# Optimization experiments

Measured on AMD Instinct MI355X. Metric: run time of the kernel, lower is better.

## Reference

```python
import jax, jax.numpy as jnp
import numpy as np

B, T, C = 4, 2048, 1024
H, D = 16, 64


def setup_inputs() -> dict:
    key = jax.random.key(0)
    ks = jax.random.split(key, 5)
    x = jax.random.normal(ks[0], (B, T, C), dtype=jnp.float32)
    Wq = jax.random.normal(ks[1], (H, C, D), dtype=jnp.float32) * (C ** -0.5)
    Wk = jax.random.normal(ks[2], (H, C, D), dtype=jnp.float32) * (C ** -0.5)
    Wv = jax.random.normal(ks[3], (H, C, D), dtype=jnp.float32) * (C ** -0.5)
    Wp = jax.random.normal(ks[4], (H * D, C), dtype=jnp.float32) * ((H * D) ** -0.5)
    bp = jnp.zeros((C,), dtype=jnp.float32)
    return {"x": x, "Wq": Wq, "Wk": Wk, "Wv": Wv, "Wp": Wp, "bp": bp}


def reference(x, Wq, Wk, Wv, Wp, bp):
    # per-head projections (bias-free): [B,H,T,D]
    q = jnp.einsum('btc,hcd->bhtd', x, Wq)
    k = jnp.einsum('btc,hcd->bhtd', x, Wk)
    v = jnp.einsum('btc,hcd->bhtd', x, Wv)
    # NOTE: source multiplies by sqrt(head_size) (faithful to original code)
    scale = jnp.asarray(D ** 0.5, x.dtype)
    att = jnp.einsum('bhtd,bhsd->bhts', q, k) * scale  # [B,H,T,T]
    causal = jnp.tril(jnp.ones((T, T), dtype=bool))
    att = jnp.where(causal, att, jnp.asarray(-jnp.inf, att.dtype))
    att = jax.nn.softmax(att, axis=-1)
    out = jnp.einsum('bhts,bhsd->bhtd', att, v)  # [B,H,T,D]
    out = out.transpose(0, 2, 1, 3).reshape(B, T, H * D)  # head concat
    return out @ Wp + bp
```

## Files before the change

kernel.cpp:

```cpp
#include <hip/hip_runtime.h>

#define B_ 4
#define T_ 2048
#define C_ 1024
#define H_ 16
#define D_ 64

typedef _Float16 f16x8 __attribute__((ext_vector_type(8)));
typedef __fp16 fp16x2 __attribute__((ext_vector_type(2)));
typedef float f32x4 __attribute__((ext_vector_type(4)));
typedef unsigned short u16x8 __attribute__((ext_vector_type(8)));

#define MFMA16 __builtin_amdgcn_mfma_f32_16x16x32_f16
#define SCALE2 11.541560327111707f

__device__ __forceinline__ unsigned pk2(float a, float b) {
    fp16x2 p = __builtin_amdgcn_cvt_pkrtz(a, b);
    return __builtin_bit_cast(unsigned, p);
}

__device__ __forceinline__ void gl_lds16(const _Float16* g, unsigned short* lds) {
    __builtin_amdgcn_global_load_lds(
        (const __attribute__((address_space(1))) unsigned int*)g,
        (__attribute__((address_space(3))) unsigned int*)lds, 16, 0, 0);
}

__global__ __launch_bounds__(256) void convx_kernel(const float* __restrict__ x,
                                                    _Float16* __restrict__ Xf) {
    size_t i = ((size_t)blockIdx.x * 256 + threadIdx.x) * 8;
    f32x4 a = *reinterpret_cast<const f32x4*>(x + i);
    f32x4 b = *reinterpret_cast<const f32x4*>(x + i + 4);
    f16x8 o;
    o[0] = (_Float16)a[0]; o[1] = (_Float16)a[1]; o[2] = (_Float16)a[2]; o[3] = (_Float16)a[3];
    o[4] = (_Float16)b[0]; o[5] = (_Float16)b[1]; o[6] = (_Float16)b[2]; o[7] = (_Float16)b[3];
    *reinterpret_cast<f16x8*>(Xf + i) = o;
}

__global__ __launch_bounds__(256) void convw_qkv_kernel(
    const float* __restrict__ Wq, const float* __restrict__ Wk, const float* __restrict__ Wv,
    _Float16* __restrict__ Wqt, _Float16* __restrict__ Wkt, _Float16* __restrict__ Wvt)
{
    __shared__ unsigned short Wl[128][72];
    const int ct = blockIdx.x, h = blockIdx.y, m = blockIdx.z;
    const float* src = (m == 0 ? Wq : (m == 1 ? Wk : Wv)) + ((size_t)h * C_ + ct * 128) * D_;
    _Float16* dst = (m == 0 ? Wqt : (m == 1 ? Wkt : Wvt));
    const int tid = threadIdx.x;
    {
        int r = tid >> 1, half = tid & 1;
        #pragma unroll
        for (int i = 0; i < 8; i++) {
            f32x4 v = *reinterpret_cast<const f32x4*>(src + (size_t)r * D_ + half * 32 + i * 4);
            #pragma unroll
            for (int j = 0; j < 4; j++)
                Wl[r][half * 32 + i * 4 + j] = __builtin_bit_cast(unsigned short, (_Float16)v[j]);
        }
    }
    __syncthreads();
    {
        int d = tid >> 2, seg = tid & 3;
        #pragma unroll
        for (int i = 0; i < 4; i++) {
            u16x8 o;
            #pragma unroll
            for (int j = 0; j < 8; j++) o[j] = Wl[seg * 32 + i * 8 + j][d];
            *reinterpret_cast<u16x8*>((unsigned short*)dst + ((size_t)h * D_ + d) * C_ + ct * 128 + seg * 32 + i * 8) = o;
        }
    }
}

__global__ __launch_bounds__(256) void convw_p_kernel(const float* __restrict__ Wp,
                                                      _Float16* __restrict__ Wpt)
{
    __shared__ unsigned short Pl[64][72];
    const int jt = blockIdx.x, kt = blockIdx.y;
    const int tid = threadIdx.x;
    {
        int r = tid >> 2, seg = tid & 3;
        #pragma unroll
        for (int i = 0; i < 4; i++) {
            f32x4 v = *reinterpret_cast<const f32x4*>(Wp + (size_t)(kt * 64 + r) * C_ + jt * 64 + seg * 16 + i * 4);
            #pragma unroll
            for (int j = 0; j < 4; j++)
                Pl[r][seg * 16 + i * 4 + j] = __builtin_bit_cast(unsigned short, (_Float16)v[j]);
        }
    }
    __syncthreads();
    {
        int jj = tid >> 2, kseg = tid & 3;
        #pragma unroll
        for (int i = 0; i < 2; i++) {
            u16x8 o;
            #pragma unroll
            for (int j = 0; j < 8; j++) o[j] = Pl[kseg * 16 + i * 8 + j][jj];
            *reinterpret_cast<u16x8*>((unsigned short*)Wpt + (size_t)(jt * 64 + jj) * C_ + kt * 64 + kseg * 16 + i * 8) = o;
        }
    }
}

__global__ __launch_bounds__(256) void qkv4_kernel(
    const _Float16* __restrict__ Xf, const _Float16* __restrict__ Wcat,
    _Float16* __restrict__ Qf, _Float16* __restrict__ Kf, _Float16* __restrict__ Vt)
{
    __shared__ unsigned short As[128 * 64];
    __shared__ unsigned short Bs[192 * 64];
    const int rt = blockIdx.x, ct = blockIdx.y;
    const int row0 = rt * 128, n0 = ct * 192;
    const int tid = threadIdx.x, wid = tid >> 6, lane = tid & 63;
    const int l15 = lane & 15, g = lane >> 4;
    const int wr = wid >> 1, wc = wid & 1;
    const int lrow = lane >> 3, lcol = (lane & 7) * 8;

    f32x4 acc[4][6];
    #pragma unroll
    for (int mi = 0; mi < 4; mi++)
        #pragma unroll
        for (int ni = 0; ni < 6; ni++) { f32x4 z = {0.f,0.f,0.f,0.f}; acc[mi][ni] = z; }

    for (int k0 = 0; k0 < C_; k0 += 64) {
        __syncthreads();
        #pragma unroll
        for (int i = 0; i < 4; i++) {
            int c = wid * 4 + i;
            gl_lds16(Xf + (size_t)(row0 + c * 8 + lrow) * C_ + k0 + lcol, &As[c * 512]);
        }
        #pragma unroll
        for (int i = 0; i < 6; i++) {
            int c = wid * 6 + i;
            gl_lds16(Wcat + (size_t)(n0 + c * 8 + lrow) * C_ + k0 + lcol, &Bs[c * 512]);
        }
        __syncthreads();
        #pragma unroll
        for (int kk = 0; kk < 2; kk++) {
            f16x8 af[4];
            #pragma unroll
            for (int mi = 0; mi < 4; mi++)
                af[mi] = *reinterpret_cast<const f16x8*>(&As[(wr * 64 + mi * 16 + l15) * 64 + kk * 32 + g * 8]);
            #pragma unroll
            for (int ni = 0; ni < 6; ni++) {
                f16x8 bf = *reinterpret_cast<const f16x8*>(&Bs[(wc * 96 + ni * 16 + l15) * 64 + kk * 32 + g * 8]);
                #pragma unroll
                for (int mi = 0; mi < 4; mi++)
                    acc[mi][ni] = MFMA16(af[mi], bf, acc[mi][ni], 0, 0, 0);
            }
        }
    }

    const int b = row0 >> 11;
    const int t0b = (row0 & (T_ - 1)) + wr * 64;
    #pragma unroll
    for (int ni = 0; ni < 6; ni++) {
        const int n = n0 + wc * 96 + ni * 16;
        const int region = n >> 10;
        const int h = (n >> 6) & 15;
        const int d0 = n & 63;
        if (region < 2) {
            _Float16* dst = region ? Kf : Qf;
            const float osc = region ? 1.0f : SCALE2;
            const size_t hb = ((size_t)(b * H_ + h)) * T_ * D_;
            #pragma unroll
            for (int mi = 0; mi < 4; mi++)
                #pragma unroll
                for (int r = 0; r < 4; r++) {
                    int t = t0b + mi * 16 + g * 4 + r;
                    dst[hb + (size_t)t * D_ + d0 + l15] = (_Float16)(acc[mi][ni][r] * osc);
                }
        } else {
            const size_t vbase = ((size_t)(b * H_ + h)) * D_ * T_;
            const int d = d0 + l15;
            #pragma unroll
            for (int mi = 0; mi < 4; mi++) {
                int t = t0b + mi * 16 + g * 4;
                uint2 w;
                w.x = pk2(acc[mi][ni][0], acc[mi][ni][1]);
                w.y = pk2(acc[mi][ni][2], acc[mi][ni][3]);
                *reinterpret_cast<uint2*>((unsigned short*)Vt + vbase + (size_t)d * T_ + t) = w;
            }
        }
    }
}

__global__ __launch_bounds__(256) void flash_kernel(
    const _Float16* __restrict__ Qf, const _Float16* __restrict__ Kf,
    const _Float16* __restrict__ Vt, _Float16* __restrict__ att)
{
    __shared__ __align__(16) unsigned short Ks[2][64 * 64];
    __shared__ __align__(16) unsigned short Vs[2][64 * 64];
    __shared__ __align__(16) unsigned short Ps[4][32 * 32];
    const int bh = blockIdx.x;
    const int p = (int)blockIdx.y;
    const int bb = bh >> 4, h = bh & 15;
    const int tid = threadIdx.x, wid = tid >> 6, lane = tid & 63;
    const int l15 = lane & 15, g = lane >> 4;

    const _Float16* Qb = Qf + (size_t)bh * T_ * D_;
    const _Float16* Kb = Kf + (size_t)bh * T_ * D_;
    const _Float16* Vb = Vt + (size_t)bh * D_ * T_;

    const int srow = lane >> 3;
    const int sunit = (lane & 7) ^ srow;
    const int r0s = wid * 16;

    char* const pbase = (char*)&Ps[wid][0];

    for (int pass = 0; pass < 2; pass++) {
        const int qt = pass ? p : (15 - p);
        const int q0 = qt * 128;
        const int qw = q0 + wid * 32;

        f16x8 qf[2][2];
        #pragma unroll
        for (int mt = 0; mt < 2; mt++)
            #pragma unroll
            for (int kk = 0; kk < 2; kk++)
                qf[mt][kk] = *reinterpret_cast<const f16x8*>(Qb + (size_t)(qw + mt * 16 + l15) * D_ + kk * 32 + g * 8);

        f32x4 accO[4][2];
        #pragma unroll
        for (int nt = 0; nt < 4; nt++)
            #pragma unroll
            for (int mt = 0; mt < 2; mt++) { f32x4 z = {0.f,0.f,0.f,0.f}; accO[nt][mt] = z; }
        float m[2] = { -1e30f, -1e30f };
        float l[2] = { 0.f, 0.f };

        const int myNt = (qw + 95) >> 6;
        const int ntB  = (q0 + 191) >> 6;

        #pragma unroll
        for (int i = 0; i < 2; i++) {
            int row = r0s + i * 8 + srow;
            gl_lds16(Kb + (size_t)row * D_ + sunit * 8, &Ks[0][(r0s + i * 8) * 64]);
            gl_lds16(Vb + (size_t)row * T_ + sunit * 8, &Vs[0][(r0s + i * 8) * 64]);
        }
        __syncthreads();

#define TILE_BODY(TI, BUF)                                                          \
    {                                                                               \
        const int kv0 = (TI) * 64;                                                  \
        if ((TI) + 1 < ntB) {                                                       \
            const int kvn = kv0 + 64;                                               \
            _Pragma("unroll")                                                       \
            for (int i = 0; i < 2; i++) {                                           \
                int row = r0s + i * 8 + srow;                                       \
                gl_lds16(Kb + (size_t)(kvn + row) * D_ + sunit * 8,                 \
                         &Ks[(BUF) ^ 1][(r0s + i * 8) * 64]);                       \
                gl_lds16(Vb + (size_t)row * T_ + kvn + sunit * 8,                   \
                         &Vs[(BUF) ^ 1][(r0s + i * 8) * 64]);                       \
            }                                                                       \
        }                                                                           \
        if ((TI) < myNt) {                                                          \
            const bool maskt = ((TI) == myNt - 1);                                  \
            const char* kbase = (const char*)&Ks[BUF][0];                           \
            const char* vbase = (const char*)&Vs[BUF][0];                           \
            f32x4 s[4][2];                                                          \
            _Pragma("unroll")                                                       \
            for (int st = 0; st < 4; st++)                                          \
                _Pragma("unroll")                                                   \
                for (int mt = 0; mt < 2; mt++) { f32x4 z = {0.f,0.f,0.f,0.f}; s[st][mt] = z; } \
            _Pragma("unroll")                                                       \
            for (int kk = 0; kk < 2; kk++) {                                        \
                f16x8 kfr[4];                                                       \
                _Pragma("unroll")                                                   \
                for (int st = 0; st < 4; st++) {                                    \
                    int row = st * 16 + l15;                                        \
                    kfr[st] = *reinterpret_cast<const f16x8*>(                      \
                        kbase + row * 128 + (((kk * 4 + g) ^ (row & 7)) * 16));     \
                }                                                                   \
                _Pragma("unroll")                                                   \
                for (int st = 0; st < 4; st++)                                      \
                    _Pragma("unroll")                                               \
                    for (int mt = 0; mt < 2; mt++)                                  \
                        s[st][mt] = MFMA16(kfr[st], qf[mt][kk], s[st][mt], 0, 0, 0);\
            }                                                                       \
            unsigned pw[2][4][2];                                                   \
            _Pragma("unroll")                                                       \
            for (int mt = 0; mt < 2; mt++) {                                        \
                const int r = mt * 16 + l15;                                        \
                const int qrow = qw + r;                                            \
                float lv[4][4];                                                     \
                float vmax = -1e30f;                                                \
                _Pragma("unroll")                                                   \
                for (int st = 0; st < 4; st++)                                      \
                    _Pragma("unroll")                                               \
                    for (int rr = 0; rr < 4; rr++) {                                \
                        float v = s[st][mt][rr];                                    \
                        if (maskt) {                                                \
                            int kv = kv0 + st * 16 + g * 4 + rr;                    \
                            v = (kv <= qrow) ? v : -1e30f;                          \
                        }                                                           \
                        lv[st][rr] = v;                                             \
                        vmax = fmaxf(vmax, v);                                      \
                    }                                                               \
                vmax = fmaxf(vmax, __shfl_xor(vmax, 16, 64));                       \
                vmax = fmaxf(vmax, __shfl_xor(vmax, 32, 64));                       \
                float mnew = fmaxf(m[mt], vmax);                                    \
                float alpha = __builtin_amdgcn_exp2f(m[mt] - mnew);                 \
                m[mt] = mnew;                                                       \
                float rs = 0.f;                                                     \
                _Pragma("unroll")                                                   \
                for (int st = 0; st < 4; st++) {                                    \
                    float p0 = __builtin_amdgcn_exp2f(lv[st][0] - mnew);            \
                    float p1 = __builtin_amdgcn_exp2f(lv[st][1] - mnew);            \
                    float p2 = __builtin_amdgcn_exp2f(lv[st][2] - mnew);            \
                    float p3 = __builtin_amdgcn_exp2f(lv[st][3] - mnew);            \
                    rs += (p0 + p1) + (p2 + p3);                                    \
                    pw[mt][st][0] = pk2(p0, p1);                                    \
                    pw[mt][st][1] = pk2(p2, p3);                                    \
                }                                                                   \
                rs += __shfl_xor(rs, 16, 64);                                       \
                rs += __shfl_xor(rs, 32, 64);                                       \
                l[mt] = l[mt] * alpha + rs;                                         \
                _Pragma("unroll")                                                   \
                for (int nt = 0; nt < 4; nt++) accO[nt][mt] *= alpha;               \
            }                                                                       \
            _Pragma("unroll")                                                       \
            for (int half = 0; half < 2; half++) {                                  \
                _Pragma("unroll")                                                   \
                for (int mt = 0; mt < 2; mt++) {                                    \
                    const int r = mt * 16 + l15;                                    \
                    const int swz = ((r >> 1) & 3) << 4;                            \
                    char* prow = pbase + r * 64;                                    \
                    _Pragma("unroll")                                               \
                    for (int stl = 0; stl < 2; stl++) {                             \
                        uint2 w;                                                    \
                        w.x = pw[mt][half * 2 + stl][0];                            \
                        w.y = pw[mt][half * 2 + stl][1];                            \
                        *reinterpret_cast<uint2*>(prow + ((stl * 32 + g * 8) ^ swz)) = w; \
                    }                                                               \
                }                                                                   \
                f16x8 pb[2];                                                        \
                _Pragma("unroll")                                                   \
                for (int mt = 0; mt < 2; mt++) {                                    \
                    const int r = mt * 16 + l15;                                    \
                    const int swz = ((r >> 1) & 3) << 4;                            \
                    pb[mt] = *reinterpret_cast<const f16x8*>(pbase + r * 64 + ((g * 16) ^ swz)); \
                }                                                                   \
                _Pragma("unroll")                                                   \
                for (int nt = 0; nt < 4; nt++) {                                    \
                    int row = nt * 16 + l15;                                        \
                    f16x8 vf = *reinterpret_cast<const f16x8*>(                     \
                        vbase + row * 128 + (((half * 4 + g) ^ (row & 7)) * 16));   \
                    _Pragma("unroll")                                               \
                    for (int mt = 0; mt < 2; mt++)                                  \
                        accO[nt][mt] = MFMA16(vf, pb[mt], accO[nt][mt], 0, 0, 0);   \
                }                                                                   \
            }                                                                       \
        }                                                                           \
        __syncthreads();                                                            \
    }

        for (int tI = 0; tI < ntB; tI += 2) {
            TILE_BODY(tI, 0)
            if (tI + 1 < ntB) {
                TILE_BODY(tI + 1, 1)
            }
        }
#undef TILE_BODY

        #pragma unroll
        for (int mt = 0; mt < 2; mt++) {
            float inv = 1.0f / l[mt];
            int t = qw + mt * 16 + l15;
            #pragma unroll
            for (int nt = 0; nt < 4; nt++) {
                f32x4 o = accO[nt][mt] * inv;
                uint2 w;
                w.x = pk2(o[0], o[1]);
                w.y = pk2(o[2], o[3]);
                size_t off = ((size_t)(bb * T_ + t)) * (H_ * D_) + h * D_ + nt * 16 + g * 4;
                *reinterpret_cast<uint2*>((unsigned short*)att + off) = w;
            }
        }
    }
}

__global__ __launch_bounds__(256) void proj2_kernel(
    const _Float16* __restrict__ att, const _Float16* __restrict__ Wpt,
    const float* __restrict__ bp, float* __restrict__ out)
{
    __shared__ unsigned short As[128 * 64];
    __shared__ unsigned short Bs[128 * 64];
    const int rt = blockIdx.x, ct = blockIdx.y;
    const int row0 = rt * 128, n0 = ct * 128;
    const int tid = threadIdx.x, wid = tid >> 6, lane = tid & 63;
    const int l15 = lane & 15, g = lane >> 4;
    const int wr = wid >> 1, wc = wid & 1;
    const int lrow = lane >> 3, lcol = (lane & 7) * 8;

    f32x4 acc[4][4];
    #pragma unroll
    for (int mi = 0; mi < 4; mi++)
        #pragma unroll
        for (int ni = 0; ni < 4; ni++) { f32x4 z = {0.f,0.f,0.f,0.f}; acc[mi][ni] = z; }

    for (int k0 = 0; k0 < C_; k0 += 64) {
        __syncthreads();
        #pragma unroll
        for (int i = 0; i < 4; i++) {
            int c = wid * 4 + i;
            gl_lds16(att + (size_t)(row0 + c * 8 + lrow) * C_ + k0 + lcol, &As[c * 512]);
            gl_lds16(Wpt + (size_t)(n0   + c * 8 + lrow) * C_ + k0 + lcol, &Bs[c * 512]);
        }
        __syncthreads();
        #pragma unroll
        for (int kk = 0; kk < 2; kk++) {
            f16x8 af[4], bf[4];
            #pragma unroll
            for (int mi = 0; mi < 4; mi++)
                af[mi] = *reinterpret_cast<const f16x8*>(&As[(wr * 64 + mi * 16 + l15) * 64 + kk * 32 + g * 8]);
            #pragma unroll
            for (int ni = 0; ni < 4; ni++)
                bf[ni] = *reinterpret_cast<const f16x8*>(&Bs[(wc * 64 + ni * 16 + l15) * 64 + kk * 32 + g * 8]);
            #pragma unroll
            for (int mi = 0; mi < 4; mi++)
                #pragma unroll
                for (int ni = 0; ni < 4; ni++)
                    acc[mi][ni] = MFMA16(af[mi], bf[ni], acc[mi][ni], 0, 0, 0);
        }
    }

    #pragma unroll
    for (int mi = 0; mi < 4; mi++)
        #pragma unroll
        for (int ni = 0; ni < 4; ni++) {
            int col = n0 + wc * 64 + ni * 16 + l15;
            float bias = bp[col];
            #pragma unroll
            for (int r = 0; r < 4; r++) {
                int row = row0 + wr * 64 + mi * 16 + g * 4 + r;
                out[(size_t)row * C_ + col] = acc[mi][ni][r] + bias;
            }
        }
}

extern "C" void kernel_launch(void* const* d_in, const int* in_sizes, int n_in,
                              void* d_out, int out_size, void* d_ws, size_t ws_size,
                              hipStream_t stream) {
    const float* x  = (const float*)d_in[0];
    const float* Wq = (const float*)d_in[1];
    const float* Wk = (const float*)d_in[2];
    const float* Wv = (const float*)d_in[3];
    const float* Wp = (const float*)d_in[4];
    const float* bp = (const float*)d_in[5];
    float* out = (float*)d_out;

    _Float16* Xf  = (_Float16*)d_ws;
    _Float16* Wqt = Xf  + (size_t)8388608;
    _Float16* Wkt = Wqt + (size_t)1048576;
    _Float16* Wvt = Wkt + (size_t)1048576;
    _Float16* Wpt = Wvt + (size_t)1048576;
    _Float16* Qf  = Wpt + (size_t)1048576;
    _Float16* Kf  = Qf  + (size_t)8388608;
    _Float16* Vt  = Kf  + (size_t)8388608;
    _Float16* att = Vt  + (size_t)8388608;

    convx_kernel<<<4096, 256, 0, stream>>>(x, Xf);
    convw_qkv_kernel<<<dim3(8, 16, 3), 256, 0, stream>>>(Wq, Wk, Wv, Wqt, Wkt, Wvt);
    convw_p_kernel<<<dim3(16, 16), 256, 0, stream>>>(Wp, Wpt);
    qkv4_kernel<<<dim3(64, 16), 256, 0, stream>>>(Xf, Wqt, Qf, Kf, Vt);
    flash_kernel<<<dim3(64, 8), 256, 0, stream>>>(Qf, Kf, Vt, att);
    proj2_kernel<<<dim3(64, 8), 256, 0, stream>>>(att, Wpt, bp, out);
}
```

Measured before the change: 195.5 us.

## Shrink flash query tile to 64 rows, doubling grid for more parallelism

The flash attention block now covers 64 query rows, one 16-row MFMA tile per wave, instead of 128 rows with two tiles per wave. The grid doubles to 64x16 with paired causal tiles (31-j and j), which raises block count and lowers register use per wave to improve occupancy and load balance. In exchange, each K/V tile loaded into LDS is reused by half as many query rows, so K/V traffic per unit of work doubles. The per-wave skip of fully masked KV tiles is removed because all waves now share the same tile count.

```diff
diff --git a/kernel.cpp b/kernel.cpp
--- a/kernel.cpp
+++ b/kernel.cpp
@@ -185,9 +185,9 @@
 {
     __shared__ __align__(16) unsigned short Ks[2][64 * 64];
     __shared__ __align__(16) unsigned short Vs[2][64 * 64];
-    __shared__ __align__(16) unsigned short Ps[4][32 * 32];
+    __shared__ __align__(16) unsigned short Ps[4][16 * 32];
     const int bh = blockIdx.x;
-    const int p = (int)blockIdx.y;
+    const int j = (int)blockIdx.y;
     const int bb = bh >> 4, h = bh & 15;
     const int tid = threadIdx.x, wid = tid >> 6, lane = tid & 63;
     const int l15 = lane & 15, g = lane >> 4;
@@ -201,29 +201,27 @@
     const int r0s = wid * 16;
 
     char* const pbase = (char*)&Ps[wid][0];
+    const int r = l15;
+    const int swz = ((r >> 1) & 3) << 4;
 
     for (int pass = 0; pass < 2; pass++) {
-        const int qt = pass ? p : (15 - p);
-        const int q0 = qt * 128;
-        const int qw = q0 + wid * 32;
-
-        f16x8 qf[2][2];
-        #pragma unroll
-        for (int mt = 0; mt < 2; mt++)
-            #pragma unroll
-            for (int kk = 0; kk < 2; kk++)
-                qf[mt][kk] = *reinterpret_cast<const f16x8*>(Qb + (size_t)(qw + mt * 16 + l15) * D_ + kk * 32 + g * 8);
-
-        f32x4 accO[4][2];
-        #pragma unroll
-        for (int nt = 0; nt < 4; nt++)
-            #pragma unroll
-            for (int mt = 0; mt < 2; mt++) { f32x4 z = {0.f,0.f,0.f,0.f}; accO[nt][mt] = z; }
-        float m[2] = { -1e30f, -1e30f };
-        float l[2] = { 0.f, 0.f };
-
-        const int myNt = (qw + 95) >> 6;
-        const int ntB  = (q0 + 191) >> 6;
+        const int s = pass ? j : (31 - j);
+        const int q0 = s * 64;
+        const int qw = q0 + wid * 16;
+        const int qrow = qw + r;
+
+        f16x8 qf[2];
+        #pragma unroll
+        for (int kk = 0; kk < 2; kk++)
+            qf[kk] = *reinterpret_cast<const f16x8*>(Qb + (size_t)(qw + l15) * D_ + kk * 32 + g * 8);
+
+        f32x4 accO[4];
+        #pragma unroll
+        for (int nt = 0; nt < 4; nt++) { f32x4 z = {0.f,0.f,0.f,0.f}; accO[nt] = z; }
+        float m = -1e30f;
+        float l = 0.f;
+
+        const int ntB = s + 1;
 
         #pragma unroll
         for (int i = 0; i < 2; i++) {
@@ -247,15 +245,13 @@
                          &Vs[(BUF) ^ 1][(r0s + i * 8) * 64]);                       \
             }                                                                       \
         }                                                                           \
-        if ((TI) < myNt) {                                                          \
-            const bool maskt = ((TI) == myNt - 1);                                  \
+        {                                                                           \
+            const bool maskt = ((TI) == ntB - 1);                                   \
             const char* kbase = (const char*)&Ks[BUF][0];                           \
             const char* vbase = (const char*)&Vs[BUF][0];                           \
-            f32x4 s[4][2];                                                          \
-            _Pragma("unroll")                                                       \
-            for (int st = 0; st < 4; st++)                                          \
-                _Pragma("unroll")                                                   \
-                for (int mt = 0; mt < 2; mt++) { f32x4 z = {0.f,0.f,0.f,0.f}; s[st][mt] = z; } \
+            f32x4 s4[4];                                                            \
+            _Pragma("unroll")                                                       \
+            for (int st = 0; st < 4; st++) { f32x4 z = {0.f,0.f,0.f,0.f}; s4[st] = z; } \
             _Pragma("unroll")                                                       \
             for (int kk = 0; kk < 2; kk++) {                                        \
                 f16x8 kfr[4];                                                       \
@@ -267,81 +263,61 @@
                 }                                                                   \
                 _Pragma("unroll")                                                   \
                 for (int st = 0; st < 4; st++)                                      \
-                    _Pragma("unroll")                                               \
-                    for (int mt = 0; mt < 2; mt++)                                  \
-                        s[st][mt] = MFMA16(kfr[st], qf[mt][kk], s[st][mt], 0, 0, 0);\
+                    s4[st] = MFMA16(kfr[st], qf[kk], s4[st], 0, 0, 0);              \
             }                                                                       \
-            unsigned pw[2][4][2];                                                   \
-            _Pragma("unroll")                                                       \
-            for (int mt = 0; mt < 2; mt++) {                                        \
-                const int r = mt * 16 + l15;                                        \
-                const int qrow = qw + r;                                            \
-                float lv[4][4];                                                     \
-                float vmax = -1e30f;                                                \
+            float lv[4][4];                                                         \
+            float vmax = -1e30f;                                                    \
+            _Pragma("unroll")                                                       \
+            for (int st = 0; st < 4; st++)                                          \
                 _Pragma("unroll")                                                   \
-                for (int st = 0; st < 4; st++)                                      \
-                    _Pragma("unroll")                                               \
-                    for (int rr = 0; rr < 4; rr++) {                                \
-                        float v = s[st][mt][rr];                                    \
-                        if (maskt) {                                                \
-                            int kv = kv0 + st * 16 + g * 4 + rr;                    \
-                            v = (kv <= qrow) ? v : -1e30f;                          \
-                        }                                                           \
-                        lv[st][rr] = v;                                             \
-                        vmax = fmaxf(vmax, v);                                      \
+                for (int rr = 0; rr < 4; rr++) {                                    \
+                    float v = s4[st][rr];                                           \
+                    if (maskt) {                                                    \
+                        int kv = kv0 + st * 16 + g * 4 + rr;                        \
+                        v = (kv <= qrow) ? v : -1e30f;                              \
                     }                                                               \
-                vmax = fmaxf(vmax, __shfl_xor(vmax, 16, 64));                       \
-                vmax = fmaxf(vmax, __shfl_xor(vmax, 32, 64));                       \
-                float mnew = fmaxf(m[mt], vmax);                                    \
-                float alpha = __builtin_amdgcn_exp2f(m[mt] - mnew);                 \
-                m[mt] = mnew;                                                       \
-                float rs = 0.f;                                                     \
-                _Pragma("unroll")                                                   \
-                for (int st = 0; st < 4; st++) {                                    \
-                    float p0 = __builtin_amdgcn_exp2f(lv[st][0] - mnew);            \
-                    float p1 = __builtin_amdgcn_exp2f(lv[st][1] - mnew);            \
-                    float p2 = __builtin_amdgcn_exp2f(lv[st][2] - mnew);            \
-                    float p3 = __builtin_amdgcn_exp2f(lv[st][3] - mnew);            \
-                    rs += (p0 + p1) + (p2 + p3);                                    \
-                    pw[mt][st][0] = pk2(p0, p1);                                    \
-                    pw[mt][st][1] = pk2(p2, p3);                                    \
+                    lv[st][rr] = v;                                                 \
+                    vmax = fmaxf(vmax, v);                                          \
                 }                                                                   \
-                rs += __shfl_xor(rs, 16, 64);                                       \
-                rs += __shfl_xor(rs, 32, 64);                                       \
-                l[mt] = l[mt] * alpha + rs;                                         \
-                _Pragma("unroll")                                                   \
-                for (int nt = 0; nt < 4; nt++) accO[nt][mt] *= alpha;               \
+            vmax = fmaxf(vmax, __shfl_xor(vmax, 16, 64));                           \
+            vmax = fmaxf(vmax, __shfl_xor(vmax, 32, 64));                           \
+            float mnew = fmaxf(m, vmax);                                            \
+            float alpha = __builtin_amdgcn_exp2f(m - mnew);                         \
+            m = mnew;                                                               \
+            float rs = 0.f;                                                         \
+            unsigned pw[4][2];                                                      \
+            _Pragma("unroll")                                                       \
+            for (int st = 0; st < 4; st++) {                                        \
+                float p0 = __builtin_amdgcn_exp2f(lv[st][0] - mnew);                \
+                float p1 = __builtin_amdgcn_exp2f(lv[st][1] - mnew);                \
+                float p2 = __builtin_amdgcn_exp2f(lv[st][2] - mnew);                \
+                float p3 = __builtin_amdgcn_exp2f(lv[st][3] - mnew);                \
+                rs += (p0 + p1) + (p2 + p3);                                        \
+                pw[st][0] = pk2(p0, p1);                                            \
+                pw[st][1] = pk2(p2, p3);                                            \
             }                                                                       \
+            rs += __shfl_xor(rs, 16, 64);                                           \
+            rs += __shfl_xor(rs, 32, 64);                                           \
+            l = l * alpha + rs;                                                     \
+            _Pragma("unroll")                                                       \
+            for (int nt = 0; nt < 4; nt++) accO[nt] *= alpha;                       \
+            char* prow = pbase + r * 64;                                            \
             _Pragma("unroll")                                                       \
             for (int half = 0; half < 2; half++) {                                  \
                 _Pragma("unroll")                                                   \
-                for (int mt = 0; mt < 2; mt++) {                                    \
-                    const int r = mt * 16 + l15;                                    \
-                    const int swz = ((r >> 1) & 3) << 4;                            \
-                    char* prow = pbase + r * 64;                                    \
-                    _Pragma("unroll")                                               \
-                    for (int stl = 0; stl < 2; stl++) {                             \
-                        uint2 w;                                                    \
-                        w.x = pw[mt][half * 2 + stl][0];                            \
-                        w.y = pw[mt][half * 2 + stl][1];                            \
-                        *reinterpret_cast<uint2*>(prow + ((stl * 32 + g * 8) ^ swz)) = w; \
-                    }                                                               \
+                for (int stl = 0; stl < 2; stl++) {                                 \
+                    uint2 w;                                                        \
+                    w.x = pw[half * 2 + stl][0];                                    \
+                    w.y = pw[half * 2 + stl][1];                                    \
+                    *reinterpret_cast<uint2*>(prow + ((stl * 32 + g * 8) ^ swz)) = w; \
                 }                                                                   \
-                f16x8 pb[2];                                                        \
-                _Pragma("unroll")                                                   \
-                for (int mt = 0; mt < 2; mt++) {                                    \
-                    const int r = mt * 16 + l15;                                    \
-                    const int swz = ((r >> 1) & 3) << 4;                            \
-                    pb[mt] = *reinterpret_cast<const f16x8*>(pbase + r * 64 + ((g * 16) ^ swz)); \
-                }                                                                   \
+                f16x8 pb = *reinterpret_cast<const f16x8*>(prow + ((g * 16) ^ swz)); \
                 _Pragma("unroll")                                                   \
                 for (int nt = 0; nt < 4; nt++) {                                    \
                     int row = nt * 16 + l15;                                        \
                     f16x8 vf = *reinterpret_cast<const f16x8*>(                     \
                         vbase + row * 128 + (((half * 4 + g) ^ (row & 7)) * 16));   \
-                    _Pragma("unroll")                                               \
-                    for (int mt = 0; mt < 2; mt++)                                  \
-                        accO[nt][mt] = MFMA16(vf, pb[mt], accO[nt][mt], 0, 0, 0);   \
+                    accO[nt] = MFMA16(vf, pb, accO[nt], 0, 0, 0);                   \
                 }                                                                   \
             }                                                                       \
         }                                                                           \
@@ -356,13 +332,12 @@
         }
 #undef TILE_BODY
 
-        #pragma unroll
-        for (int mt = 0; mt < 2; mt++) {
-            float inv = 1.0f / l[mt];
-            int t = qw + mt * 16 + l15;
+        {
+            float inv = 1.0f / l;
+            int t = qw + l15;
             #pragma unroll
             for (int nt = 0; nt < 4; nt++) {
-                f32x4 o = accO[nt][mt] * inv;
+                f32x4 o = accO[nt] * inv;
                 uint2 w;
                 w.x = pk2(o[0], o[1]);
                 w.y = pk2(o[2], o[3]);
@@ -457,6 +432,6 @@
     convw_qkv_kernel<<<dim3(8, 16, 3), 256, 0, stream>>>(Wq, Wk, Wv, Wqt, Wkt, Wvt);
     convw_p_kernel<<<dim3(16, 16), 256, 0, stream>>>(Wp, Wpt);
     qkv4_kernel<<<dim3(64, 16), 256, 0, stream>>>(Xf, Wqt, Qf, Kf, Vt);
-    flash_kernel<<<dim3(64, 8), 256, 0, stream>>>(Qf, Kf, Vt, att);
+    flash_kernel<<<dim3(64, 16), 256, 0, stream>>>(Qf, Kf, Vt, att);
     proj2_kernel<<<dim3(64, 8), 256, 0, stream>>>(att, Wpt, bp, out);
 }
```

New measurement: 191.2 us. 1.02x faster.

## Give each flash block one query tile and skip rescale when max is unchanged

Applied to the files above, without the earlier changes.

The flash kernel previously paired a heavy and a light query tile in two passes per block to balance the causal work. Now each block handles a single query tile (descending order by blockIdx.y), and the grid doubles to 1024 blocks for more parallelism and better latency hiding. The online-softmax rescale of accO and l is skipped when no lane's max increases, and LDS fragment offsets are precomputed once per thread. Dropping the pairing relies on the hardware scheduler to balance uneven causal work, and the precomputed offsets may raise register pressure.

```diff
diff --git a/kernel.cpp b/kernel.cpp
--- a/kernel.cpp
+++ b/kernel.cpp
@@ -187,10 +187,12 @@
     __shared__ __align__(16) unsigned short Vs[2][64 * 64];
     __shared__ __align__(16) unsigned short Ps[4][32 * 32];
     const int bh = blockIdx.x;
-    const int p = (int)blockIdx.y;
+    const int qt = 15 - (int)blockIdx.y;
     const int bb = bh >> 4, h = bh & 15;
     const int tid = threadIdx.x, wid = tid >> 6, lane = tid & 63;
     const int l15 = lane & 15, g = lane >> 4;
+    const int q0 = qt * 128;
+    const int qw = q0 + wid * 32;
 
     const _Float16* Qb = Qf + (size_t)bh * T_ * D_;
     const _Float16* Kb = Kf + (size_t)bh * T_ * D_;
@@ -200,38 +202,48 @@
     const int sunit = (lane & 7) ^ srow;
     const int r0s = wid * 16;
 
+    int lsoff[2][4];
+    #pragma unroll
+    for (int kk = 0; kk < 2; kk++)
+        #pragma unroll
+        for (int st = 0; st < 4; st++) {
+            int row = st * 16 + l15;
+            lsoff[kk][st] = row * 128 + (((kk * 4 + g) ^ (row & 7)) * 16);
+        }
+    int pbs[2], psw[2];
+    #pragma unroll
+    for (int mt = 0; mt < 2; mt++) {
+        int r = mt * 16 + l15;
+        pbs[mt] = r * 64;
+        psw[mt] = ((r >> 1) & 3) << 4;
+    }
     char* const pbase = (char*)&Ps[wid][0];
 
-    for (int pass = 0; pass < 2; pass++) {
-        const int qt = pass ? p : (15 - p);
-        const int q0 = qt * 128;
-        const int qw = q0 + wid * 32;
-
-        f16x8 qf[2][2];
-        #pragma unroll
-        for (int mt = 0; mt < 2; mt++)
-            #pragma unroll
-            for (int kk = 0; kk < 2; kk++)
-                qf[mt][kk] = *reinterpret_cast<const f16x8*>(Qb + (size_t)(qw + mt * 16 + l15) * D_ + kk * 32 + g * 8);
-
-        f32x4 accO[4][2];
-        #pragma unroll
-        for (int nt = 0; nt < 4; nt++)
-            #pragma unroll
-            for (int mt = 0; mt < 2; mt++) { f32x4 z = {0.f,0.f,0.f,0.f}; accO[nt][mt] = z; }
-        float m[2] = { -1e30f, -1e30f };
-        float l[2] = { 0.f, 0.f };
-
-        const int myNt = (qw + 95) >> 6;
-        const int ntB  = (q0 + 191) >> 6;
-
-        #pragma unroll
-        for (int i = 0; i < 2; i++) {
-            int row = r0s + i * 8 + srow;
-            gl_lds16(Kb + (size_t)row * D_ + sunit * 8, &Ks[0][(r0s + i * 8) * 64]);
-            gl_lds16(Vb + (size_t)row * T_ + sunit * 8, &Vs[0][(r0s + i * 8) * 64]);
-        }
-        __syncthreads();
+    f16x8 qf[2][2];
+    #pragma unroll
+    for (int mt = 0; mt < 2; mt++)
+        #pragma unroll
+        for (int kk = 0; kk < 2; kk++)
+            qf[mt][kk] = *reinterpret_cast<const f16x8*>(Qb + (size_t)(qw + mt * 16 + l15) * D_ + kk * 32 + g * 8);
+
+    f32x4 accO[4][2];
+    #pragma unroll
+    for (int nt = 0; nt < 4; nt++)
+        #pragma unroll
+        for (int mt = 0; mt < 2; mt++) { f32x4 z = {0.f,0.f,0.f,0.f}; accO[nt][mt] = z; }
+    float m[2] = { -1e30f, -1e30f };
+    float l[2] = { 0.f, 0.f };
+
+    const int myNt = (qw + 95) >> 6;
+    const int ntB  = (q0 + 191) >> 6;
+
+    #pragma unroll
+    for (int i = 0; i < 2; i++) {
+        int row = r0s + i * 8 + srow;
+        gl_lds16(Kb + (size_t)row * D_ + sunit * 8, &Ks[0][(r0s + i * 8) * 64]);
+        gl_lds16(Vb + (size_t)row * T_ + sunit * 8, &Vs[0][(r0s + i * 8) * 64]);
+    }
+    __syncthreads();
 
 #define TILE_BODY(TI, BUF)                                                          \
     {                                                                               \
@@ -260,11 +272,8 @@
             for (int kk = 0; kk < 2; kk++) {                                        \
                 f16x8 kfr[4];                                                       \
                 _Pragma("unroll")                                                   \
-                for (int st = 0; st < 4; st++) {                                    \
-                    int row = st * 16 + l15;                                        \
-                    kfr[st] = *reinterpret_cast<const f16x8*>(                      \
-                        kbase + row * 128 + (((kk * 4 + g) ^ (row & 7)) * 16));     \
-                }                                                                   \
+                for (int st = 0; st < 4; st++)                                      \
+                    kfr[st] = *reinterpret_cast<const f16x8*>(kbase + lsoff[kk][st]); \
                 _Pragma("unroll")                                                   \
                 for (int st = 0; st < 4; st++)                                      \
                     _Pragma("unroll")                                               \
@@ -274,8 +283,7 @@
             unsigned pw[2][4][2];                                                   \
             _Pragma("unroll")                                                       \
             for (int mt = 0; mt < 2; mt++) {                                        \
-                const int r = mt * 16 + l15;                                        \
-                const int qrow = qw + r;                                            \
+                const int qrow = qw + mt * 16 + l15;                                \
                 float lv[4][4];                                                     \
                 float vmax = -1e30f;                                                \
                 _Pragma("unroll")                                                   \
@@ -292,53 +300,49 @@
                     }                                                               \
                 vmax = fmaxf(vmax, __shfl_xor(vmax, 16, 64));                       \
                 vmax = fmaxf(vmax, __shfl_xor(vmax, 32, 64));                       \
-                float mnew = fmaxf(m[mt], vmax);                                    \
-                float alpha = __builtin_amdgcn_exp2f(m[mt] - mnew);                 \
-                m[mt] = mnew;                                                       \
+                if (__any(vmax > m[mt])) {                                          \
+                    float mnew = fmaxf(m[mt], vmax);                                \
+                    float alpha = __builtin_amdgcn_exp2f(m[mt] - mnew);             \
+                    m[mt] = mnew;                                                   \
+                    l[mt] *= alpha;                                                 \
+                    _Pragma("unroll")                                               \
+                    for (int nt = 0; nt < 4; nt++) accO[nt][mt] *= alpha;           \
+                }                                                                   \
                 float rs = 0.f;                                                     \
                 _Pragma("unroll")                                                   \
                 for (int st = 0; st < 4; st++) {                                    \
-                    float p0 = __builtin_amdgcn_exp2f(lv[st][0] - mnew);            \
-                    float p1 = __builtin_amdgcn_exp2f(lv[st][1] - mnew);            \
-                    float p2 = __builtin_amdgcn_exp2f(lv[st][2] - mnew);            \
-                    float p3 = __builtin_amdgcn_exp2f(lv[st][3] - mnew);            \
+                    float p0 = __builtin_amdgcn_exp2f(lv[st][0] - m[mt]);           \
+                    float p1 = __builtin_amdgcn_exp2f(lv[st][1] - m[mt]);           \
+                    float p2 = __builtin_amdgcn_exp2f(lv[st][2] - m[mt]);           \
+                    float p3 = __builtin_amdgcn_exp2f(lv[st][3] - m[mt]);           \
                     rs += (p0 + p1) + (p2 + p3);                                    \
                     pw[mt][st][0] = pk2(p0, p1);                                    \
                     pw[mt][st][1] = pk2(p2, p3);                                    \
                 }                                                                   \
                 rs += __shfl_xor(rs, 16, 64);                                       \
                 rs += __shfl_xor(rs, 32, 64);                                       \
-                l[mt] = l[mt] * alpha + rs;                                         \
-                _Pragma("unroll")                                                   \
-                for (int nt = 0; nt < 4; nt++) accO[nt][mt] *= alpha;               \
+                l[mt] += rs;                                                        \
             }                                                                       \
             _Pragma("unroll")                                                       \
             for (int half = 0; half < 2; half++) {                                  \
                 _Pragma("unroll")                                                   \
                 for (int mt = 0; mt < 2; mt++) {                                    \
-                    const int r = mt * 16 + l15;                                    \
-                    const int swz = ((r >> 1) & 3) << 4;                            \
-                    char* prow = pbase + r * 64;                                    \
+                    char* prow = pbase + pbs[mt];                                   \
                     _Pragma("unroll")                                               \
                     for (int stl = 0; stl < 2; stl++) {                             \
                         uint2 w;                                                    \
                         w.x = pw[mt][half * 2 + stl][0];                            \
                         w.y = pw[mt][half * 2 + stl][1];                            \
-                        *reinterpret_cast<uint2*>(prow + ((stl * 32 + g * 8) ^ swz)) = w; \
+                        *reinterpret_cast<uint2*>(prow + ((stl * 32 + g * 8) ^ psw[mt])) = w; \
                     }                                                               \
                 }                                                                   \
                 f16x8 pb[2];                                                        \
                 _Pragma("unroll")                                                   \
-                for (int mt = 0; mt < 2; mt++) {                                    \
-                    const int r = mt * 16 + l15;                                    \
-                    const int swz = ((r >> 1) & 3) << 4;                            \
-                    pb[mt] = *reinterpret_cast<const f16x8*>(pbase + r * 64 + ((g * 16) ^ swz)); \
-                }                                                                   \
+                for (int mt = 0; mt < 2; mt++)                                      \
+                    pb[mt] = *reinterpret_cast<const f16x8*>(pbase + pbs[mt] + ((g * 16) ^ psw[mt])); \
                 _Pragma("unroll")                                                   \
                 for (int nt = 0; nt < 4; nt++) {                                    \
-                    int row = nt * 16 + l15;                                        \
-                    f16x8 vf = *reinterpret_cast<const f16x8*>(                     \
-                        vbase + row * 128 + (((half * 4 + g) ^ (row & 7)) * 16));   \
+                    f16x8 vf = *reinterpret_cast<const f16x8*>(vbase + lsoff[half][nt]); \
                     _Pragma("unroll")                                               \
                     for (int mt = 0; mt < 2; mt++)                                  \
                         accO[nt][mt] = MFMA16(vf, pb[mt], accO[nt][mt], 0, 0, 0);   \
@@ -348,27 +352,26 @@
         __syncthreads();                                                            \
     }
 
-        for (int tI = 0; tI < ntB; tI += 2) {
-            TILE_BODY(tI, 0)
-            if (tI + 1 < ntB) {
-                TILE_BODY(tI + 1, 1)
-            }
-        }
+    for (int tI = 0; tI < ntB; tI += 2) {
+        TILE_BODY(tI, 0)
+        if (tI + 1 < ntB) {
+            TILE_BODY(tI + 1, 1)
+        }
+    }
 #undef TILE_BODY
 
-        #pragma unroll
-        for (int mt = 0; mt < 2; mt++) {
-            float inv = 1.0f / l[mt];
-            int t = qw + mt * 16 + l15;
-            #pragma unroll
-            for (int nt = 0; nt < 4; nt++) {
-                f32x4 o = accO[nt][mt] * inv;
-                uint2 w;
-                w.x = pk2(o[0], o[1]);
-                w.y = pk2(o[2], o[3]);
-                size_t off = ((size_t)(bb * T_ + t)) * (H_ * D_) + h * D_ + nt * 16 + g * 4;
-                *reinterpret_cast<uint2*>((unsigned short*)att + off) = w;
-            }
+    #pragma unroll
+    for (int mt = 0; mt < 2; mt++) {
+        float inv = 1.0f / l[mt];
+        int t = qw + mt * 16 + l15;
+        #pragma unroll
+        for (int nt = 0; nt < 4; nt++) {
+            f32x4 o = accO[nt][mt] * inv;
+            uint2 w;
+            w.x = pk2(o[0], o[1]);
+            w.y = pk2(o[2], o[3]);
+            size_t off = ((size_t)(bb * T_ + t)) * (H_ * D_) + h * D_ + nt * 16 + g * 4;
+            *reinterpret_cast<uint2*>((unsigned short*)att + off) = w;
         }
     }
 }
@@ -457,6 +460,6 @@
     convw_qkv_kernel<<<dim3(8, 16, 3), 256, 0, stream>>>(Wq, Wk, Wv, Wqt, Wkt, Wvt);
     convw_p_kernel<<<dim3(16, 16), 256, 0, stream>>>(Wp, Wpt);
     qkv4_kernel<<<dim3(64, 16), 256, 0, stream>>>(Xf, Wqt, Qf, Kf, Vt);
-    flash_kernel<<<dim3(64, 8), 256, 0, stream>>>(Qf, Kf, Vt, att);
+    flash_kernel<<<dim3(64, 16), 256, 0, stream>>>(Qf, Kf, Vt, att);
     proj2_kernel<<<dim3(64, 8), 256, 0, stream>>>(att, Wpt, bp, out);
 }
```

New measurement: 196.0 us. Within noise of the previous version (+0.3%).

## Split flash kernel into one query tile per block and single-buffer V

Applied to the files above, without the earlier changes.

Drops the two-pass pairing of query tiles per block and launches one block per 128-row query tile, doubling the grid. V becomes a single LDS buffer loaded at the start of each tile and overlapped with the QK^T and softmax work, with an added barrier before the PV product. This cuts LDS use, which may raise occupancy. The online-softmax rescale of the accumulator and row sum is skipped when no lane's row max increased. Costs are an extra barrier per tile, less prefetch lead time for V, and uneven causal work across blocks.

```diff
diff --git a/kernel.cpp b/kernel.cpp
--- a/kernel.cpp
+++ b/kernel.cpp
@@ -184,13 +184,15 @@
     const _Float16* __restrict__ Vt, _Float16* __restrict__ att)
 {
     __shared__ __align__(16) unsigned short Ks[2][64 * 64];
-    __shared__ __align__(16) unsigned short Vs[2][64 * 64];
+    __shared__ __align__(16) unsigned short Vs[64 * 64];
     __shared__ __align__(16) unsigned short Ps[4][32 * 32];
     const int bh = blockIdx.x;
-    const int p = (int)blockIdx.y;
+    const int qt = 15 - (int)blockIdx.y;
     const int bb = bh >> 4, h = bh & 15;
     const int tid = threadIdx.x, wid = tid >> 6, lane = tid & 63;
     const int l15 = lane & 15, g = lane >> 4;
+    const int q0 = qt * 128;
+    const int qw = q0 + wid * 32;
 
     const _Float16* Qb = Qf + (size_t)bh * T_ * D_;
     const _Float16* Kb = Kf + (size_t)bh * T_ * D_;
@@ -201,41 +203,42 @@
     const int r0s = wid * 16;
 
     char* const pbase = (char*)&Ps[wid][0];
-
-    for (int pass = 0; pass < 2; pass++) {
-        const int qt = pass ? p : (15 - p);
-        const int q0 = qt * 128;
-        const int qw = q0 + wid * 32;
-
-        f16x8 qf[2][2];
-        #pragma unroll
-        for (int mt = 0; mt < 2; mt++)
-            #pragma unroll
-            for (int kk = 0; kk < 2; kk++)
-                qf[mt][kk] = *reinterpret_cast<const f16x8*>(Qb + (size_t)(qw + mt * 16 + l15) * D_ + kk * 32 + g * 8);
-
-        f32x4 accO[4][2];
-        #pragma unroll
-        for (int nt = 0; nt < 4; nt++)
-            #pragma unroll
-            for (int mt = 0; mt < 2; mt++) { f32x4 z = {0.f,0.f,0.f,0.f}; accO[nt][mt] = z; }
-        float m[2] = { -1e30f, -1e30f };
-        float l[2] = { 0.f, 0.f };
-
-        const int myNt = (qw + 95) >> 6;
-        const int ntB  = (q0 + 191) >> 6;
-
-        #pragma unroll
-        for (int i = 0; i < 2; i++) {
-            int row = r0s + i * 8 + srow;
-            gl_lds16(Kb + (size_t)row * D_ + sunit * 8, &Ks[0][(r0s + i * 8) * 64]);
-            gl_lds16(Vb + (size_t)row * T_ + sunit * 8, &Vs[0][(r0s + i * 8) * 64]);
-        }
-        __syncthreads();
+    const char* const vbase = (const char*)&Vs[0];
+
+    f16x8 qf[2][2];
+    #pragma unroll
+    for (int mt = 0; mt < 2; mt++)
+        #pragma unroll
+        for (int kk = 0; kk < 2; kk++)
+            qf[mt][kk] = *reinterpret_cast<const f16x8*>(Qb + (size_t)(qw + mt * 16 + l15) * D_ + kk * 32 + g * 8);
+
+    f32x4 accO[4][2];
+    #pragma unroll
+    for (int nt = 0; nt < 4; nt++)
+        #pragma unroll
+        for (int mt = 0; mt < 2; mt++) { f32x4 z = {0.f,0.f,0.f,0.f}; accO[nt][mt] = z; }
+    float m[2] = { -1e30f, -1e30f };
+    float l[2] = { 0.f, 0.f };
+
+    const int myNt = (qw + 95) >> 6;
+    const int ntB  = (q0 + 191) >> 6;
+
+    #pragma unroll
+    for (int i = 0; i < 2; i++) {
+        int row = r0s + i * 8 + srow;
+        gl_lds16(Kb + (size_t)row * D_ + sunit * 8, &Ks[0][(r0s + i * 8) * 64]);
+    }
+    __syncthreads();
 
 #define TILE_BODY(TI, BUF)                                                          \
     {                                                                               \
         const int kv0 = (TI) * 64;                                                  \
+                            \
+        _Pragma("unroll")                                                           \
+        for (int i = 0; i < 2; i++) {                                               \
+            int row = r0s + i * 8 + srow;                                           \
+            gl_lds16(Vb + (size_t)row * T_ + kv0 + sunit * 8, &Vs[(r0s + i * 8) * 64]); \
+        }                                                                           \
         if ((TI) + 1 < ntB) {                                                       \
             const int kvn = kv0 + 64;                                               \
             _Pragma("unroll")                                                       \
@@ -243,14 +246,12 @@
                 int row = r0s + i * 8 + srow;                                       \
                 gl_lds16(Kb + (size_t)(kvn + row) * D_ + sunit * 8,                 \
                          &Ks[(BUF) ^ 1][(r0s + i * 8) * 64]);                       \
-                gl_lds16(Vb + (size_t)row * T_ + kvn + sunit * 8,                   \
-                         &Vs[(BUF) ^ 1][(r0s + i * 8) * 64]);                       \
             }                                                                       \
         }                                                                           \
+        unsigned pw[2][4][2];                                                       \
         if ((TI) < myNt) {                                                          \
             const bool maskt = ((TI) == myNt - 1);                                  \
             const char* kbase = (const char*)&Ks[BUF][0];                           \
-            const char* vbase = (const char*)&Vs[BUF][0];                           \
             f32x4 s[4][2];                                                          \
             _Pragma("unroll")                                                       \
             for (int st = 0; st < 4; st++)                                          \
@@ -271,11 +272,9 @@
                     for (int mt = 0; mt < 2; mt++)                                  \
                         s[st][mt] = MFMA16(kfr[st], qf[mt][kk], s[st][mt], 0, 0, 0);\
             }                                                                       \
-            unsigned pw[2][4][2];                                                   \
             _Pragma("unroll")                                                       \
             for (int mt = 0; mt < 2; mt++) {                                        \
-                const int r = mt * 16 + l15;                                        \
-                const int qrow = qw + r;                                            \
+                const int qrow = qw + mt * 16 + l15;                                \
                 float lv[4][4];                                                     \
                 float vmax = -1e30f;                                                \
                 _Pragma("unroll")                                                   \
@@ -292,26 +291,32 @@
                     }                                                               \
                 vmax = fmaxf(vmax, __shfl_xor(vmax, 16, 64));                       \
                 vmax = fmaxf(vmax, __shfl_xor(vmax, 32, 64));                       \
-                float mnew = fmaxf(m[mt], vmax);                                    \
-                float alpha = __builtin_amdgcn_exp2f(m[mt] - mnew);                 \
-                m[mt] = mnew;                                                       \
+                if (__any(vmax > m[mt])) {                                          \
+                    float mnew = fmaxf(m[mt], vmax);                                \
+                    float alpha = __builtin_amdgcn_exp2f(m[mt] - mnew);             \
+                    m[mt] = mnew;                                                   \
+                    l[mt] *= alpha;                                                 \
+                    _Pragma("unroll")                                               \
+                    for (int nt = 0; nt < 4; nt++) accO[nt][mt] *= alpha;           \
+                }                                                                   \
                 float rs = 0.f;                                                     \
                 _Pragma("unroll")                                                   \
                 for (int st = 0; st < 4; st++) {                                    \
-                    float p0 = __builtin_amdgcn_exp2f(lv[st][0] - mnew);            \
-                    float p1 = __builtin_amdgcn_exp2f(lv[st][1] - mnew);            \
-                    float p2 = __builtin_amdgcn_exp2f(lv[st][2] - mnew);            \
-                    float p3 = __builtin_amdgcn_exp2f(lv[st][3] - mnew);            \
+                    float p0 = __builtin_amdgcn_exp2f(lv[st][0] - m[mt]);           \
+                    float p1 = __builtin_amdgcn_exp2f(lv[st][1] - m[mt]);           \
+                    float p2 = __builtin_amdgcn_exp2f(lv[st][2] - m[mt]);           \
+                    float p3 = __builtin_amdgcn_exp2f(lv[st][3] - m[mt]);           \
                     rs += (p0 + p1) + (p2 + p3);                                    \
                     pw[mt][st][0] = pk2(p0, p1);                                    \
                     pw[mt][st][1] = pk2(p2, p3);                                    \
                 }                                                                   \
                 rs += __shfl_xor(rs, 16, 64);                                       \
                 rs += __shfl_xor(rs, 32, 64);                                       \
-                l[mt] = l[mt] * alpha + rs;                                         \
-                _Pragma("unroll")                                                   \
-                for (int nt = 0; nt < 4; nt++) accO[nt][mt] *= alpha;               \
+                l[mt] += rs;                                                        \
             }                                                                       \
+        }                                                                           \
+        __syncthreads();                          \
+        if ((TI) < myNt) {                                                          \
             _Pragma("unroll")                                                       \
             for (int half = 0; half < 2; half++) {                                  \
                 _Pragma("unroll")                                                   \
@@ -345,30 +350,29 @@
                 }                                                                   \
             }                                                                       \
         }                                                                           \
-        __syncthreads();                                                            \
-    }
-
-        for (int tI = 0; tI < ntB; tI += 2) {
-            TILE_BODY(tI, 0)
-            if (tI + 1 < ntB) {
-                TILE_BODY(tI + 1, 1)
-            }
-        }
+        __syncthreads();                                \
+    }
+
+    for (int tI = 0; tI < ntB; tI += 2) {
+        TILE_BODY(tI, 0)
+        if (tI + 1 < ntB) {
+            TILE_BODY(tI + 1, 1)
+        }
+    }
 #undef TILE_BODY
 
-        #pragma unroll
-        for (int mt = 0; mt < 2; mt++) {
-            float inv = 1.0f / l[mt];
-            int t = qw + mt * 16 + l15;
-            #pragma unroll
-            for (int nt = 0; nt < 4; nt++) {
-                f32x4 o = accO[nt][mt] * inv;
-                uint2 w;
-                w.x = pk2(o[0], o[1]);
-                w.y = pk2(o[2], o[3]);
-                size_t off = ((size_t)(bb * T_ + t)) * (H_ * D_) + h * D_ + nt * 16 + g * 4;
-                *reinterpret_cast<uint2*>((unsigned short*)att + off) = w;
-            }
+    #pragma unroll
+    for (int mt = 0; mt < 2; mt++) {
+        float inv = 1.0f / l[mt];
+        int t = qw + mt * 16 + l15;
+        #pragma unroll
+        for (int nt = 0; nt < 4; nt++) {
+            f32x4 o = accO[nt][mt] * inv;
+            uint2 w;
+            w.x = pk2(o[0], o[1]);
+            w.y = pk2(o[2], o[3]);
+            size_t off = ((size_t)(bb * T_ + t)) * (H_ * D_) + h * D_ + nt * 16 + g * 4;
+            *reinterpret_cast<uint2*>((unsigned short*)att + off) = w;
         }
     }
 }
@@ -457,6 +461,6 @@
     convw_qkv_kernel<<<dim3(8, 16, 3), 256, 0, stream>>>(Wq, Wk, Wv, Wqt, Wkt, Wvt);
     convw_p_kernel<<<dim3(16, 16), 256, 0, stream>>>(Wp, Wpt);
     qkv4_kernel<<<dim3(64, 16), 256, 0, stream>>>(Xf, Wqt, Qf, Kf, Vt);
-    flash_kernel<<<dim3(64, 8), 256, 0, stream>>>(Qf, Kf, Vt, att);
+    flash_kernel<<<dim3(64, 16), 256, 0, stream>>>(Qf, Kf, Vt, att);
     proj2_kernel<<<dim3(64, 8), 256, 0, stream>>>(att, Wpt, bp, out);
 }
```

New measurement: 198.1 us. About the same (+1.3%).
